# Kernel optimization log

Hardware: AMD Instinct MI355X
Metric: run time of the kernel (lower is better)

## Reference

```python
import jax, jax.numpy as jnp
import numpy as np
import math

D_MODEL = 1024
NUM_HEADS = 16
D_K = D_MODEL // NUM_HEADS
THETA = 10000.0
BATCH = 2
SEQ = 2048


def _trunc_normal(key, shape, std):
    # truncated normal in [-3std, 3std], matching torch.nn.init.trunc_normal_
    return jax.random.truncated_normal(key, -3.0, 3.0, shape, jnp.float32) * std


def setup_inputs() -> dict:
    key = jax.random.key(0)
    kx, kq, kk, kv, ko = jax.random.split(key, 5)
    std = math.sqrt(2.0 / (D_MODEL + D_MODEL))
    return {
        "x": jax.random.normal(kx, (BATCH, SEQ, D_MODEL), jnp.float32),
        "Wq": _trunc_normal(kq, (D_MODEL, D_MODEL), std),
        "Wk": _trunc_normal(kk, (D_MODEL, D_MODEL), std),
        "Wv": _trunc_normal(kv, (D_MODEL, D_MODEL), std),
        "Wo": _trunc_normal(ko, (D_MODEL, D_MODEL), std),
    }


def _apply_rope(t):
    # t: [B, H, S, d_k]; positions = arange(S)
    S = t.shape[-2]
    inv_freq = 1.0 / THETA ** (jnp.arange(0, D_K, 2, dtype=jnp.float32) / D_K)
    ang = jnp.arange(S, dtype=jnp.float32)[:, None] * inv_freq[None, :]  # [S, d_k/2]
    cos, sin = jnp.cos(ang), jnp.sin(ang)
    t1 = t[..., ::2]
    t2 = t[..., 1::2]
    r1 = t1 * cos - t2 * sin
    r2 = t1 * sin + t2 * cos
    # interleave back: even indices <- r1, odd <- r2
    out = jnp.stack([r1, r2], axis=-1).reshape(t.shape)
    return out


def reference(x, Wq, Wk, Wv, Wo):
    B, S, _ = x.shape
    def proj(W):
        return (x @ W.T).reshape(B, S, NUM_HEADS, D_K).transpose(0, 2, 1, 3)
    q = _apply_rope(proj(Wq))
    k = _apply_rope(proj(Wk))
    v = proj(Wv)
    scores = jnp.einsum('bhqd,bhkd->bhqk', q, k) / math.sqrt(D_K)
    causal = jnp.tril(jnp.ones((S, S), dtype=bool))
    scores = jnp.where(causal, scores, -jnp.inf)
    attn = jax.nn.softmax(scores, axis=-1)
    ctx = jnp.einsum('bhqk,bhkd->bhqd', attn, v)  # [B,H,S,d_k]
    ctx = ctx.transpose(0, 2, 1, 3).reshape(B, S, D_MODEL)
    return ctx @ Wo.T
```

## Files before the change

kernel.cpp:

```cpp
#include <hip/hip_runtime.h>
#include <hip/hip_bf16.h>


typedef __attribute__((ext_vector_type(8))) short bf16x8;
typedef __attribute__((ext_vector_type(4))) short bf16x4;
typedef __attribute__((ext_vector_type(4))) float f32x4;

#define D_MODEL 1024
#define SEQ     2048
#define NHEAD   16
#define DK      64
#define EXP_BIAS 16.0f
#define ROPE_LN 0.28782313663f

__device__ __forceinline__ f32x4 mfma16(bf16x8 a, bf16x8 b, f32x4 c) {
    return __builtin_amdgcn_mfma_f32_16x16x32_bf16(a, b, c, 0, 0, 0);
}

__device__ __forceinline__ void load_lds16(const __hip_bfloat16* g, __hip_bfloat16* l) {
    __builtin_amdgcn_global_load_lds((const __attribute__((address_space(1))) void*)g,
                                     (__attribute__((address_space(3))) void*)l,
                                     16, 0, 0);
}

__device__ __forceinline__ void cvt8(const float* p, __hip_bfloat16* dst) {
    const float4 f0 = *(const float4*)p;
    const float4 f1 = *(const float4*)(p + 4);
    alignas(16) __hip_bfloat16 t[8] = {
        __float2bfloat16(f0.x), __float2bfloat16(f0.y),
        __float2bfloat16(f0.z), __float2bfloat16(f0.w),
        __float2bfloat16(f1.x), __float2bfloat16(f1.y),
        __float2bfloat16(f1.z), __float2bfloat16(f1.w)};
    *(bf16x8*)dst = *(const bf16x8*)t;
}

__global__ __launch_bounds__(256) void cvt5_k(const float* __restrict__ wq,
                                              const float* __restrict__ wk,
                                              const float* __restrict__ wv,
                                              const float* __restrict__ wo,
                                              const float* __restrict__ x,
                                              __hip_bfloat16* __restrict__ dw,
                                              __hip_bfloat16* __restrict__ dwo,
                                              __hip_bfloat16* __restrict__ dx) {
    const int id = blockIdx.x;
    const float* s;
    __hip_bfloat16* d;
    int off;
    if (id < 1536)      { const int w = id >> 9; s = (w == 0) ? wq : (w == 1 ? wk : wv);
                          d = dw + (size_t)w * 1024 * 1024; off = (id & 511) * 2048; }
    else if (id < 2048) { s = wo; d = dwo; off = (id - 1536) * 2048; }
    else                { s = x;  d = dx;  off = (id - 2048) * 2048; }
    const int i = off + threadIdx.x * 8;
    alignas(16) __hip_bfloat16 t[8];
    cvt8(s + i, t);
    *(bf16x8*)(d + i) = *(const bf16x8*)t;
}

__global__ __launch_bounds__(256) void cvt3_k(const float* __restrict__ s0,
                                              const float* __restrict__ s1,
                                              const float* __restrict__ s2,
                                              __hip_bfloat16* __restrict__ d0,
                                              __hip_bfloat16* __restrict__ d1,
                                              __hip_bfloat16* __restrict__ d2) {
    const float* s = (blockIdx.y == 0) ? s0 : (blockIdx.y == 1 ? s1 : s2);
    __hip_bfloat16* d = (blockIdx.y == 0) ? d0 : (blockIdx.y == 1 ? d1 : d2);
    const int i = (blockIdx.x * 256 + threadIdx.x) * 8;
    alignas(16) __hip_bfloat16 t[8];
    cvt8(s + i, t);
    *(bf16x8*)(d + i) = *(const bf16x8*)t;
}

__device__ __forceinline__ void qkv_epilogue(f32x4 (&acc)[4][4], int wsel,
                                             int bm, int bn, int wave,
                                             int quad, int l15,
                                             __hip_bfloat16* Cq,
                                             __hip_bfloat16* Ck,
                                             __hip_bfloat16* Vt) {
    if (wsel < 2) {
        __hip_bfloat16* C = (wsel == 0) ? Cq : Ck;
        const float qscale = (wsel == 0) ? 0.125f : 1.0f;
        const float sgn = (l15 & 1) ? 1.0f : -1.0f;
#pragma unroll
        for (int j = 0; j < 4; ++j) {
            const int ipair = (j * 16 + l15) >> 1;
            const float invf = __expf(-(float)ipair * ROPE_LN);
            const int col = bn + (wave & 1) * 64 + j * 16 + l15;
#pragma unroll
            for (int i = 0; i < 4; ++i)
#pragma unroll
                for (int r = 0; r < 4; ++r) {
                    const int row = bm + (wave >> 1) * 64 + i * 16 + quad * 4 + r;
                    const int s = row & (SEQ - 1);
                    float sn, cs;
                    __sincosf((float)s * invf, &sn, &cs);
                    const float v = acc[i][j][r];
                    const float part = __shfl_xor(v, 1);
                    const float out = (v * cs + part * (sgn * sn)) * qscale;
                    C[(size_t)row * 1024 + col] = __float2bfloat16(out);
                }
        }
    } else {
#pragma unroll
        for (int i = 0; i < 4; ++i)
#pragma unroll
            for (int j = 0; j < 4; ++j) {
                const int col  = bn + (wave & 1) * 64 + j * 16 + l15;
                const int hh   = col >> 6, dd = col & 63;
                const int row0 = bm + (wave >> 1) * 64 + i * 16 + quad * 4;
                const int bb   = row0 >> 11, s0 = row0 & 2047;
                alignas(8) __hip_bfloat16 t4[4] = {
                    __float2bfloat16(acc[i][j][0]), __float2bfloat16(acc[i][j][1]),
                    __float2bfloat16(acc[i][j][2]), __float2bfloat16(acc[i][j][3])};
                *(uint2*)&Vt[((size_t)(bb * 16 + hh) * 64 + dd) * 2048 + s0] =
                    *(const uint2*)t4;
            }
    }
}

__global__ __launch_bounds__(256) void gemm_qkv_bf(const __hip_bfloat16* __restrict__ X,
                                                   const __hip_bfloat16* __restrict__ W,
                                                   __hip_bfloat16* __restrict__ Cq,
                                                   __hip_bfloat16* __restrict__ Ck,
                                                   __hip_bfloat16* __restrict__ Vt) {
    __shared__ alignas(16) __hip_bfloat16 a_lds[2][128 * 32];
    __shared__ alignas(16) __hip_bfloat16 b_lds[2][128 * 32];

    const int tid  = threadIdx.x;
    const int wave = tid >> 6;
    const int lane = tid & 63;
    const int quad = lane >> 4;
    const int l15  = lane & 15;

    const int wsel = blockIdx.x >> 3;
    const int bn   = (blockIdx.x & 7) * 128;
    const int bm   = blockIdx.y * 128;

    const __hip_bfloat16* B = W + (size_t)wsel * 1024 * 1024;

    f32x4 acc[4][4] = {};

    auto stage = [&](int buf, int k0) {
#pragma unroll
        for (int c = 0; c < 2; ++c) {
            const int chunk = (wave * 2 + c) * 64 + lane;
            const int row = chunk >> 2;
            const int col = (chunk & 3) * 8;
            load_lds16(&X[(size_t)(bm + row) * 1024 + k0 + col],
                       &a_lds[buf][(wave * 2 + c) * 512]);
            load_lds16(&B[(size_t)(bn + row) * 1024 + k0 + col],
                       &b_lds[buf][(wave * 2 + c) * 512]);
        }
    };

    stage(0, 0);
    __syncthreads();

    for (int k0 = 0; k0 < 1024; k0 += 32) {
        const int buf = (k0 >> 5) & 1;
        if (k0 + 32 < 1024) stage(buf ^ 1, k0 + 32);

        bf16x8 af[4], bfr[4];
#pragma unroll
        for (int i = 0; i < 4; ++i)
            af[i] = *(const bf16x8*)&a_lds[buf][((wave >> 1) * 64 + i * 16 + l15) * 32 + quad * 8];
#pragma unroll
        for (int j = 0; j < 4; ++j)
            bfr[j] = *(const bf16x8*)&b_lds[buf][((wave & 1) * 64 + j * 16 + l15) * 32 + quad * 8];
#pragma unroll
        for (int i = 0; i < 4; ++i)
#pragma unroll
            for (int j = 0; j < 4; ++j)
                acc[i][j] = mfma16(af[i], bfr[j], acc[i][j]);

        __syncthreads();
    }

    qkv_epilogue(acc, wsel, bm, bn, wave, quad, l15, Cq, Ck, Vt);
}

__global__ __launch_bounds__(256) void gemm_qkv_f32(const float* __restrict__ X,
                                                    const __hip_bfloat16* __restrict__ W,
                                                    __hip_bfloat16* __restrict__ Cq,
                                                    __hip_bfloat16* __restrict__ Ck,
                                                    __hip_bfloat16* __restrict__ Vt) {
    __shared__ alignas(16) __hip_bfloat16 a_lds[128 * 32];
    __shared__ alignas(16) __hip_bfloat16 b_lds[128 * 32];

    const int tid  = threadIdx.x;
    const int wave = tid >> 6;
    const int lane = tid & 63;
    const int quad = lane >> 4;
    const int l15  = lane & 15;

    const int wsel = blockIdx.x >> 3;
    const int bn   = (blockIdx.x & 7) * 128;
    const int bm   = blockIdx.y * 128;

    const __hip_bfloat16* B = W + (size_t)wsel * 1024 * 1024;

    f32x4 acc[4][4] = {};

    for (int k0 = 0; k0 < 1024; k0 += 32) {
        __syncthreads();
#pragma unroll
        for (int c = 0; c < 2; ++c) {
            const int e   = (c * 256 + tid) * 8;
            const int row = e >> 5;
            const int col = e & 31;
            cvt8(&X[(size_t)(bm + row) * 1024 + k0 + col], &a_lds[e]);
        }
#pragma unroll
        for (int c = 0; c < 2; ++c) {
            const int chunk = (wave * 2 + c) * 64 + lane;
            const int row = chunk >> 2;
            const int col = (chunk & 3) * 8;
            load_lds16(&B[(size_t)(bn + row) * 1024 + k0 + col],
                       &b_lds[(wave * 2 + c) * 512]);
        }
        __syncthreads();

        bf16x8 af[4], bfr[4];
#pragma unroll
        for (int i = 0; i < 4; ++i)
            af[i] = *(const bf16x8*)&a_lds[((wave >> 1) * 64 + i * 16 + l15) * 32 + quad * 8];
#pragma unroll
        for (int j = 0; j < 4; ++j)
            bfr[j] = *(const bf16x8*)&b_lds[((wave & 1) * 64 + j * 16 + l15) * 32 + quad * 8];
#pragma unroll
        for (int i = 0; i < 4; ++i)
#pragma unroll
            for (int j = 0; j < 4; ++j)
                acc[i][j] = mfma16(af[i], bfr[j], acc[i][j]);
    }

    qkv_epilogue(acc, wsel, bm, bn, wave, quad, l15, Cq, Ck, Vt);
}

__global__ __launch_bounds__(256) void gemm_o(const __hip_bfloat16* __restrict__ A,
                                              const __hip_bfloat16* __restrict__ B,
                                              float* __restrict__ C) {
    __shared__ alignas(16) __hip_bfloat16 a_lds[2][128 * 32];
    __shared__ alignas(16) __hip_bfloat16 b_lds[2][64 * 32];

    const int tid  = threadIdx.x;
    const int wave = tid >> 6;
    const int lane = tid & 63;
    const int quad = lane >> 4;
    const int l15  = lane & 15;

    const int bn = blockIdx.x * 64;
    const int bm = blockIdx.y * 128;

    f32x4 acc[2][4] = {};

    auto stage = [&](int buf, int k0) {
#pragma unroll
        for (int c = 0; c < 2; ++c) {
            const int chunk = (wave * 2 + c) * 64 + lane;
            const int row = chunk >> 2;
            const int col = (chunk & 3) * 8;
            load_lds16(&A[(size_t)(bm + row) * 1024 + k0 + col],
                       &a_lds[buf][(wave * 2 + c) * 512]);
        }
        {
            const int chunk = wave * 64 + lane;
            const int row = chunk >> 2;
            const int col = (chunk & 3) * 8;
            load_lds16(&B[(size_t)(bn + row) * 1024 + k0 + col],
                       &b_lds[buf][wave * 512]);
        }
    };

    stage(0, 0);
    __syncthreads();

    for (int k0 = 0; k0 < 1024; k0 += 32) {
        const int buf = (k0 >> 5) & 1;
        if (k0 + 32 < 1024) stage(buf ^ 1, k0 + 32);

        bf16x8 af[2], bfr[4];
#pragma unroll
        for (int i = 0; i < 2; ++i)
            af[i] = *(const bf16x8*)&a_lds[buf][(wave * 32 + i * 16 + l15) * 32 + quad * 8];
#pragma unroll
        for (int j = 0; j < 4; ++j)
            bfr[j] = *(const bf16x8*)&b_lds[buf][(j * 16 + l15) * 32 + quad * 8];
#pragma unroll
        for (int i = 0; i < 2; ++i)
#pragma unroll
            for (int j = 0; j < 4; ++j)
                acc[i][j] = mfma16(af[i], bfr[j], acc[i][j]);

        __syncthreads();
    }

#pragma unroll
    for (int i = 0; i < 2; ++i)
#pragma unroll
        for (int j = 0; j < 4; ++j)
#pragma unroll
            for (int r = 0; r < 4; ++r) {
                const int row = bm + wave * 32 + i * 16 + quad * 4 + r;
                const int col = bn + j * 16 + l15;
                C[(size_t)row * 1024 + col] = acc[i][j][r];
            }
}

__global__ __launch_bounds__(256, 4) void attn_k(const __hip_bfloat16* Q,
                                                 const __hip_bfloat16* K,
                                                 const __hip_bfloat16* Vt,
                                                 __hip_bfloat16* O) {
    __shared__ alignas(16) __hip_bfloat16 k_s[2][64 * 72];
    __shared__ alignas(16) __hip_bfloat16 vt_s[2][64 * 72];

    const int tid  = threadIdx.x;
    const int wave = tid >> 6;
    const int lane = tid & 63;
    const int quad = lane >> 4;
    const int l15  = lane & 15;

    const int hw = blockIdx.x;
    const int j  = hw >> 3;
    const int g  = j >> 5;
    const int m  = j & 31;
    const int bh = (hw & 7) * 4 + g;
    const int mm = (g >= 2) ? ((m + 8) & 31) : m;
    const int qt = (g & 1) ? mm : (31 - mm);
    const int b  = bh >> 4;
    const int h  = bh & 15;
    const int q0 = qt * 64;

    const int r0 = tid >> 3;
    const int d8 = (tid & 7) * 8;
    const int vp0 = ((d8 >> 5) << 5) + (((d8 & 15) >> 2) << 3) + (((d8 >> 4) & 1) << 2);
    const int d4  = d8 + 4;
    const int vp1 = ((d4 >> 5) << 5) + (((d4 & 15) >> 2) << 3) + (((d4 >> 4) & 1) << 2);

    const size_t vtBase = (size_t)bh * (64 * 2048);
    const size_t baseK0 = ((size_t)(b * SEQ)) * D_MODEL + h * DK;

#pragma unroll
    for (int c = 0; c < 2; ++c) {
        const int row = r0 + c * 32;
        const uint4 kv = *(const uint4*)&K[baseK0 + (size_t)row * D_MODEL + d8];
        const uint4 vv = *(const uint4*)&Vt[vtBase + (size_t)row * 2048 + d8];
        *(uint4*)&k_s[0][row * 72 + d8] = kv;
        uint2 lo, hi;
        lo.x = vv.x; lo.y = vv.y; hi.x = vv.z; hi.y = vv.w;
        *(uint2*)&vt_s[0][row * 72 + vp0] = lo;
        *(uint2*)&vt_s[0][row * 72 + vp1] = hi;
    }

    bf16x8 qa0, qa1;
    {
        const size_t baseQ = ((size_t)(b * SEQ + q0 + wave * 16 + l15)) * D_MODEL + h * DK;
        qa0 = *(const bf16x8*)&Q[baseQ + quad * 8];
        qa1 = *(const bf16x8*)&Q[baseQ + 32 + quad * 8];
    }
    __syncthreads();

    float l4[4] = {0.f, 0.f, 0.f, 0.f};
    f32x4 o_acc[4] = {};

    for (int kt = 0; kt < qt; ++kt) {
        const int buf = kt & 1;

        uint4 kr0, kr1, vr0, vr1;
        {
            const size_t baseK = baseK0 + (size_t)(kt + 1) * 64 * D_MODEL;
            const size_t baseV = vtBase + (size_t)(kt + 1) * 64;
            kr0 = *(const uint4*)&K[baseK + (size_t)r0 * D_MODEL + d8];
            kr1 = *(const uint4*)&K[baseK + (size_t)(r0 + 32) * D_MODEL + d8];
            vr0 = *(const uint4*)&Vt[baseV + (size_t)r0 * 2048 + d8];
            vr1 = *(const uint4*)&Vt[baseV + (size_t)(r0 + 32) * 2048 + d8];
        }

        alignas(16) __hip_bfloat16 pk0[8], pk1[8];
#pragma unroll
        for (int t = 0; t < 4; ++t) {
            __hip_bfloat16* dst = (t < 2) ? pk0 : pk1;
            const int zo = (t & 1) * 4;
            f32x4 a = {};
            __builtin_amdgcn_s_setprio(1);
            const bf16x8 kb0 = *(const bf16x8*)&k_s[buf][(t * 16 + l15) * 72 + quad * 8];
            a = mfma16(kb0, qa0, a);
            const bf16x8 kb1 = *(const bf16x8*)&k_s[buf][(t * 16 + l15) * 72 + 32 + quad * 8];
            a = mfma16(kb1, qa1, a);
            __builtin_amdgcn_s_setprio(0);
#pragma unroll
            for (int r = 0; r < 4; ++r) {
                const float pv = __expf(a[r] - EXP_BIAS);
                l4[r] += pv;
                dst[zo + r] = __float2bfloat16(pv);
            }
        }
        const bf16x8 pa0 = *(const bf16x8*)pk0;
        const bf16x8 pa1 = *(const bf16x8*)pk1;

        __builtin_amdgcn_s_setprio(1);
#pragma unroll
        for (int ks = 0; ks < 2; ++ks) {
            const bf16x8 pa = ks ? pa1 : pa0;
#pragma unroll
            for (int t2 = 0; t2 < 4; ++t2) {
                const bf16x8 vv = *(const bf16x8*)
                    &vt_s[buf][(t2 * 16 + l15) * 72 + ks * 32 + quad * 8];
                o_acc[t2] = mfma16(pa, vv, o_acc[t2]);
            }
        }
        __builtin_amdgcn_s_setprio(0);

        *(uint4*)&k_s[buf ^ 1][r0 * 72 + d8] = kr0;
        *(uint4*)&k_s[buf ^ 1][(r0 + 32) * 72 + d8] = kr1;
        {
            uint2 lo0, hi0, lo1, hi1;
            lo0.x = vr0.x; lo0.y = vr0.y; hi0.x = vr0.z; hi0.y = vr0.w;
            lo1.x = vr1.x; lo1.y = vr1.y; hi1.x = vr1.z; hi1.y = vr1.w;
            *(uint2*)&vt_s[buf ^ 1][r0 * 72 + vp0] = lo0;
            *(uint2*)&vt_s[buf ^ 1][r0 * 72 + vp1] = hi0;
            *(uint2*)&vt_s[buf ^ 1][(r0 + 32) * 72 + vp0] = lo1;
            *(uint2*)&vt_s[buf ^ 1][(r0 + 32) * 72 + vp1] = hi1;
        }

        __syncthreads();
    }

    {
        const int buf = qt & 1;
        alignas(16) __hip_bfloat16 pk0[8], pk1[8];
#pragma unroll
        for (int t = 0; t < 4; ++t) {
            __hip_bfloat16* dst = (t < 2) ? pk0 : pk1;
            const int zo = (t & 1) * 4;
            if (t > wave) {
#pragma unroll
                for (int r = 0; r < 4; ++r) dst[zo + r] = __float2bfloat16(0.0f);
                continue;
            }
            f32x4 a = {};
            const bf16x8 kb0 = *(const bf16x8*)&k_s[buf][(t * 16 + l15) * 72 + quad * 8];
            a = mfma16(kb0, qa0, a);
            const bf16x8 kb1 = *(const bf16x8*)&k_s[buf][(t * 16 + l15) * 72 + 32 + quad * 8];
            a = mfma16(kb1, qa1, a);
#pragma unroll
            for (int r = 0; r < 4; ++r) {
                float v = a[r];
                if (t == wave && (quad * 4 + r > l15)) v = -1e30f;
                const float pv = __expf(v - EXP_BIAS);
                l4[r] += pv;
                dst[zo + r] = __float2bfloat16(pv);
            }
        }
        const bf16x8 pa0 = *(const bf16x8*)pk0;
        const bf16x8 pa1 = *(const bf16x8*)pk1;

#pragma unroll
        for (int ks = 0; ks < 2; ++ks) {
            if (ks == 1 && wave < 2) continue;
            const bf16x8 pa = ks ? pa1 : pa0;
#pragma unroll
            for (int t2 = 0; t2 < 4; ++t2) {
                const bf16x8 vv = *(const bf16x8*)
                    &vt_s[buf][(t2 * 16 + l15) * 72 + ks * 32 + quad * 8];
                o_acc[t2] = mfma16(pa, vv, o_acc[t2]);
            }
        }
    }

    float l_loc = (l4[0] + l4[1]) + (l4[2] + l4[3]);
    l_loc += __shfl_xor(l_loc, 16);
    l_loc += __shfl_xor(l_loc, 32);
    float lr[4];
#pragma unroll
    for (int r = 0; r < 4; ++r) lr[r] = __shfl(l_loc, quad * 4 + r);

#pragma unroll
    for (int t2 = 0; t2 < 4; ++t2)
#pragma unroll
        for (int r = 0; r < 4; ++r) {
            const int row = q0 + wave * 16 + quad * 4 + r;
            const int d   = t2 * 16 + l15;
            O[((size_t)(b * SEQ + row)) * D_MODEL + h * DK + d] =
                __float2bfloat16(o_acc[t2][r] / lr[r]);
        }
}

extern "C" void kernel_launch(void* const* d_in, const int* in_sizes, int n_in,
                              void* d_out, int out_size, void* d_ws, size_t ws_size,
                              hipStream_t stream) {
    const float* x  = (const float*)d_in[0];
    const float* Wq = (const float*)d_in[1];
    const float* Wk = (const float*)d_in[2];
    const float* Wv = (const float*)d_in[3];
    const float* Wo = (const float*)d_in[4];

    const size_t MT = (size_t)4096 * 1024;
    const size_t WT = (size_t)1024 * 1024;
    __hip_bfloat16* Qw = (__hip_bfloat16*)d_ws;
    __hip_bfloat16* Vt = Qw + MT;
    __hip_bfloat16* Wb = (__hip_bfloat16*)d_out;
    __hip_bfloat16* Kw = (__hip_bfloat16*)((char*)d_out + 8 * 1024 * 1024);

    const bool big = ws_size >= (size_t)26 * 1024 * 1024;

    if (big) {
        __hip_bfloat16* xb  = Qw + 2 * MT;
        __hip_bfloat16* WoB = (__hip_bfloat16*)((char*)d_ws + 24 * 1024 * 1024);
        cvt5_k<<<4096, 256, 0, stream>>>(Wq, Wk, Wv, Wo, x, Wb, WoB, xb);
        gemm_qkv_bf<<<dim3(24, 32), 256, 0, stream>>>(xb, Wb, Qw, Kw, Vt);
        attn_k<<<dim3(1024), 256, 0, stream>>>(Qw, Kw, Vt, Qw);
        gemm_o<<<dim3(16, 32), 256, 0, stream>>>(Qw, WoB, (float*)d_out);
    } else {
        __hip_bfloat16* WoB = Vt;
        cvt3_k<<<dim3(512, 3), 256, 0, stream>>>(Wq, Wk, Wv, Wb, Wb + WT, Wb + 2 * WT);
        gemm_qkv_f32<<<dim3(24, 32), 256, 0, stream>>>(x, Wb, Qw, Kw, Vt);
        attn_k<<<dim3(1024), 256, 0, stream>>>(Qw, Kw, Vt, Qw);
        cvt3_k<<<dim3(512, 1), 256, 0, stream>>>(Wo, Wo, Wo, WoB, WoB, WoB);
        gemm_o<<<dim3(16, 32), 256, 0, stream>>>(Qw, WoB, (float*)d_out);
    }
}
```

Measured before the change: 192.1 us.

## Swizzle QKV GEMM LDS, pipeline with vmcnt waits, split RoPE into kernel

The bf16 QKV GEMM now XOR-swizzles its LDS layout to avoid bank conflicts. It replaces the per-iteration __syncthreads with a two-buffer loop that uses explicit vmcnt waits and barriers, so global-to-LDS loads overlap with MFMA. RoPE and the Q scaling move out of the GEMM epilogue into a separate vectorized rope_k kernel, which removes per-element sincos and shuffles from the GEMM. The cost is one extra launch and an extra read and write pass over Q and K, plus rounding to bf16 before RoPE is applied.

```diff
diff --git a/kernel.cpp b/kernel.cpp
--- a/kernel.cpp
+++ b/kernel.cpp
@@ -11,7 +11,6 @@
 #define NHEAD   16
 #define DK      64
 #define EXP_BIAS 16.0f
-#define ROPE_LN 0.28782313663f
 
 __device__ __forceinline__ f32x4 mfma16(bf16x8 a, bf16x8 b, f32x4 c) {
     return __builtin_amdgcn_mfma_f32_16x16x32_bf16(a, b, c, 0, 0, 0);
@@ -78,27 +77,16 @@
                                              __hip_bfloat16* Vt) {
     if (wsel < 2) {
         __hip_bfloat16* C = (wsel == 0) ? Cq : Ck;
-        const float qscale = (wsel == 0) ? 0.125f : 1.0f;
-        const float sgn = (l15 & 1) ? 1.0f : -1.0f;
-#pragma unroll
-        for (int j = 0; j < 4; ++j) {
-            const int ipair = (j * 16 + l15) >> 1;
-            const float invf = __expf(-(float)ipair * ROPE_LN);
-            const int col = bn + (wave & 1) * 64 + j * 16 + l15;
-#pragma unroll
-            for (int i = 0; i < 4; ++i)
+#pragma unroll
+        for (int i = 0; i < 4; ++i)
+#pragma unroll
+            for (int j = 0; j < 4; ++j)
 #pragma unroll
                 for (int r = 0; r < 4; ++r) {
                     const int row = bm + (wave >> 1) * 64 + i * 16 + quad * 4 + r;
-                    const int s = row & (SEQ - 1);
-                    float sn, cs;
-                    __sincosf((float)s * invf, &sn, &cs);
-                    const float v = acc[i][j][r];
-                    const float part = __shfl_xor(v, 1);
-                    const float out = (v * cs + part * (sgn * sn)) * qscale;
-                    C[(size_t)row * 1024 + col] = __float2bfloat16(out);
+                    const int col = bn + (wave & 1) * 64 + j * 16 + l15;
+                    C[(size_t)row * 1024 + col] = __float2bfloat16(acc[i][j][r]);
                 }
-        }
     } else {
 #pragma unroll
         for (int i = 0; i < 4; ++i)
@@ -135,44 +123,64 @@
     const int bn   = (blockIdx.x & 7) * 128;
     const int bm   = blockIdx.y * 128;
 
-    const __hip_bfloat16* B = W + (size_t)wsel * 1024 * 1024;
+    const __hip_bfloat16* Bw = W + (size_t)wsel * 1024 * 1024;
 
     f32x4 acc[4][4] = {};
 
+    const int chunk0 = (wave * 2 + 0) * 64 + lane;
+    const int chunk1 = (wave * 2 + 1) * 64 + lane;
+    const int row0 = chunk0 >> 2, c0 = chunk0 & 3;
+    const int row1 = chunk1 >> 2, c1 = chunk1 & 3;
+    const int col0 = (c0 ^ (row0 & 3)) * 8;
+    const int col1 = (c1 ^ (row1 & 3)) * 8;
+
     auto stage = [&](int buf, int k0) {
-#pragma unroll
-        for (int c = 0; c < 2; ++c) {
-            const int chunk = (wave * 2 + c) * 64 + lane;
-            const int row = chunk >> 2;
-            const int col = (chunk & 3) * 8;
-            load_lds16(&X[(size_t)(bm + row) * 1024 + k0 + col],
-                       &a_lds[buf][(wave * 2 + c) * 512]);
-            load_lds16(&B[(size_t)(bn + row) * 1024 + k0 + col],
-                       &b_lds[buf][(wave * 2 + c) * 512]);
-        }
+        load_lds16(&X [(size_t)(bm + row0) * 1024 + k0 + col0], &a_lds[buf][(wave * 2 + 0) * 512]);
+        load_lds16(&Bw[(size_t)(bn + row0) * 1024 + k0 + col0], &b_lds[buf][(wave * 2 + 0) * 512]);
+        load_lds16(&X [(size_t)(bm + row1) * 1024 + k0 + col1], &a_lds[buf][(wave * 2 + 1) * 512]);
+        load_lds16(&Bw[(size_t)(bn + row1) * 1024 + k0 + col1], &b_lds[buf][(wave * 2 + 1) * 512]);
     };
 
-    stage(0, 0);
-    __syncthreads();
-
-    for (int k0 = 0; k0 < 1024; k0 += 32) {
-        const int buf = (k0 >> 5) & 1;
-        if (k0 + 32 < 1024) stage(buf ^ 1, k0 + 32);
-
+    const int sw8 = (quad ^ (l15 & 3)) * 8;
+
+    auto compute = [&](int buf) {
         bf16x8 af[4], bfr[4];
 #pragma unroll
         for (int i = 0; i < 4; ++i)
-            af[i] = *(const bf16x8*)&a_lds[buf][((wave >> 1) * 64 + i * 16 + l15) * 32 + quad * 8];
+            af[i] = *(const bf16x8*)&a_lds[buf][((wave >> 1) * 64 + i * 16 + l15) * 32 + sw8];
 #pragma unroll
         for (int j = 0; j < 4; ++j)
-            bfr[j] = *(const bf16x8*)&b_lds[buf][((wave & 1) * 64 + j * 16 + l15) * 32 + quad * 8];
+            bfr[j] = *(const bf16x8*)&b_lds[buf][((wave & 1) * 64 + j * 16 + l15) * 32 + sw8];
 #pragma unroll
         for (int i = 0; i < 4; ++i)
 #pragma unroll
             for (int j = 0; j < 4; ++j)
                 acc[i][j] = mfma16(af[i], bfr[j], acc[i][j]);
-
-        __syncthreads();
+    };
+
+    stage(0, 0);
+    stage(1, 32);
+
+#pragma unroll 1
+    for (int tt = 0; tt < 16; ++tt) {
+        const int k0 = tt * 64;
+
+        asm volatile("s_waitcnt vmcnt(4)" ::: "memory");
+        __builtin_amdgcn_s_barrier();
+        __builtin_amdgcn_sched_barrier(0);
+        compute(0);
+        __builtin_amdgcn_sched_barrier(0);
+        __builtin_amdgcn_s_barrier();
+        if (tt < 15) stage(0, k0 + 64);
+
+        if (tt < 15) { asm volatile("s_waitcnt vmcnt(4)" ::: "memory"); }
+        else         { asm volatile("s_waitcnt vmcnt(0)" ::: "memory"); }
+        __builtin_amdgcn_s_barrier();
+        __builtin_amdgcn_sched_barrier(0);
+        compute(1);
+        __builtin_amdgcn_sched_barrier(0);
+        __builtin_amdgcn_s_barrier();
+        if (tt < 15) stage(1, k0 + 96);
     }
 
     qkv_epilogue(acc, wsel, bm, bn, wave, quad, l15, Cq, Ck, Vt);
@@ -304,6 +312,40 @@
                 const int col = bn + j * 16 + l15;
                 C[(size_t)row * 1024 + col] = acc[i][j][r];
             }
+}
+
+__global__ __launch_bounds__(256) void rope_k(__hip_bfloat16* Q, __hip_bfloat16* K) {
+    const int idx = blockIdx.x * 256 + threadIdx.x;
+    const int row = idx >> 7;
+    const int g   = idx & 127;
+    const int col = g * 8;
+    const int s   = row & (SEQ - 1);
+    const int i0  = (g & 7) * 4;
+
+    float sn[4], cs[4];
+#pragma unroll
+    for (int z = 0; z < 4; ++z) {
+        const float ang = (float)s * __expf(-(float)(i0 + z) * 0.28782313663f);
+        __sincosf(ang, &sn[z], &cs[z]);
+    }
+
+    const size_t o = (size_t)row * D_MODEL + col;
+    alignas(16) __hip_bfloat16 q8[8], k8[8];
+    *(uint4*)q8 = *(const uint4*)&Q[o];
+    *(uint4*)k8 = *(const uint4*)&K[o];
+#pragma unroll
+    for (int z = 0; z < 4; ++z) {
+        const float q1 = __bfloat162float(q8[2 * z]);
+        const float q2 = __bfloat162float(q8[2 * z + 1]);
+        q8[2 * z]     = __float2bfloat16((q1 * cs[z] - q2 * sn[z]) * 0.125f);
+        q8[2 * z + 1] = __float2bfloat16((q1 * sn[z] + q2 * cs[z]) * 0.125f);
+        const float k1 = __bfloat162float(k8[2 * z]);
+        const float k2 = __bfloat162float(k8[2 * z + 1]);
+        k8[2 * z]     = __float2bfloat16(k1 * cs[z] - k2 * sn[z]);
+        k8[2 * z + 1] = __float2bfloat16(k1 * sn[z] + k2 * cs[z]);
+    }
+    *(uint4*)&Q[o] = *(const uint4*)q8;
+    *(uint4*)&K[o] = *(const uint4*)k8;
 }
 
 __global__ __launch_bounds__(256, 4) void attn_k(const __hip_bfloat16* Q,
@@ -508,12 +550,14 @@
         __hip_bfloat16* WoB = (__hip_bfloat16*)((char*)d_ws + 24 * 1024 * 1024);
         cvt5_k<<<4096, 256, 0, stream>>>(Wq, Wk, Wv, Wo, x, Wb, WoB, xb);
         gemm_qkv_bf<<<dim3(24, 32), 256, 0, stream>>>(xb, Wb, Qw, Kw, Vt);
+        rope_k<<<(4096 * 128) / 256, 256, 0, stream>>>(Qw, Kw);
         attn_k<<<dim3(1024), 256, 0, stream>>>(Qw, Kw, Vt, Qw);
         gemm_o<<<dim3(16, 32), 256, 0, stream>>>(Qw, WoB, (float*)d_out);
     } else {
         __hip_bfloat16* WoB = Vt;
         cvt3_k<<<dim3(512, 3), 256, 0, stream>>>(Wq, Wk, Wv, Wb, Wb + WT, Wb + 2 * WT);
         gemm_qkv_f32<<<dim3(24, 32), 256, 0, stream>>>(x, Wb, Qw, Kw, Vt);
+        rope_k<<<(4096 * 128) / 256, 256, 0, stream>>>(Qw, Kw);
         attn_k<<<dim3(1024), 256, 0, stream>>>(Qw, Kw, Vt, Qw);
         cvt3_k<<<dim3(512, 1), 256, 0, stream>>>(Wo, Wo, Wo, WoB, WoB, WoB);
         gemm_o<<<dim3(16, 32), 256, 0, stream>>>(Qw, WoB, (float*)d_out);
```

After: 184.6 us. 1.04x faster.
